# Kernel tuning notes

Hardware: AMD Instinct MI355X
Metric: run time of the kernel (lower is better)

## Reference

```python
import jax, jax.numpy as jnp
import numpy as np

PATCH = 8
MASK_RATIO = 0.75
B, H, W, C = 64, 512, 512, 3
NPH, NPW = H // PATCH, W // PATCH          # 64, 64
NP_TOT = NPH * NPW                          # 4096
NUM_MASK = int(NP_TOT * MASK_RATIO)         # 3072


def setup_inputs() -> dict:
    key = jax.random.key(0)
    k_img, k_perm = jax.random.split(key)
    images = jax.random.normal(k_img, (B, H, W, C), dtype=jnp.float32)
    # random-without-replacement masked patch indices per image (tf.random.shuffle(idx)[:num_mask])
    perm_keys = jax.random.split(k_perm, B)
    perms = jax.vmap(lambda k: jax.random.permutation(k, NP_TOT))(perm_keys)
    mask_indices = perms[:, :NUM_MASK].astype(jnp.int32)  # [B, NUM_MASK]
    return {"images": images, "mask_indices": mask_indices}


def reference(images, mask_indices):
    # Build per-image flat patch mask: ones with zeros scattered at mask_indices.
    b = images.shape[0]
    mask_flat = jnp.ones((b, NP_TOT), dtype=images.dtype)
    mask_flat = mask_flat.at[jnp.arange(b)[:, None], mask_indices].set(0.0)
    # [B, NPH, NPW] -> nearest-neighbor upsample to [B, H, W, 1] by patch repetition
    mask = mask_flat.reshape(b, NPH, NPW)
    mask = jnp.repeat(jnp.repeat(mask, PATCH, axis=1), PATCH, axis=2)[..., None]
    return images * mask
```

## Files before the change

kernel.cpp:

```cpp
#include <hip/hip_runtime.h>

#define BATCH    64
#define HEIGHT   512
#define WIDTH    512
#define CHAN     3
#define PATCH    8
#define NPH      64
#define NPW      64
#define NP_TOT   4096
#define NUM_MASK 3072

#define PER_IMG4 (HEIGHT * WIDTH * CHAN / 4)
#define PER_ROW4 (WIDTH * CHAN / 4)
#define TOTAL4   (BATCH * PER_IMG4)

typedef float f32x4 __attribute__((ext_vector_type(4)));

__global__ __launch_bounds__(256) void rm_build_mask(
        const int* __restrict__ mask_indices,
        unsigned char* __restrict__ mask) {
    const int b = blockIdx.x;
    const int t = threadIdx.x;

    uint4 ones = make_uint4(0x01010101u, 0x01010101u, 0x01010101u, 0x01010101u);
    reinterpret_cast<uint4*>(mask + b * NP_TOT)[t] = ones;
    __syncthreads();

    const int* __restrict__ idx = mask_indices + b * NUM_MASK;
    unsigned char* __restrict__ m = mask + b * NP_TOT;
#pragma unroll
    for (int j = 0; j < 12; ++j) {
        m[idx[t + j * 256]] = (unsigned char)0;
    }
}

__global__ __launch_bounds__(256) void rm_apply_mask(
        const f32x4* __restrict__ in,
        f32x4* __restrict__ out,
        const unsigned char* __restrict__ mask) {
    const int tid = blockIdx.x * blockDim.x + threadIdx.x;
    const int b  = tid / PER_IMG4;
    const int r  = tid - b * PER_IMG4;
    const int y  = r / PER_ROW4;
    const int x4 = r - y * PER_ROW4;
    const int px = x4 / 6;
    const int py = y >> 3;
    const unsigned char m = mask[b * NP_TOT + (py << 6) + px];
    f32x4 v = (f32x4)(0.f, 0.f, 0.f, 0.f);
    if (m) v = __builtin_nontemporal_load(&in[tid]);
    __builtin_nontemporal_store(v, &out[tid]);
}

extern "C" void kernel_launch(void* const* d_in, const int* in_sizes, int n_in,
                              void* d_out, int out_size, void* d_ws, size_t ws_size,
                              hipStream_t stream) {
    const float* images       = (const float*)d_in[0];
    const int*   mask_indices = (const int*)d_in[1];
    float*       out          = (float*)d_out;
    unsigned char* mask       = (unsigned char*)d_ws;

    rm_build_mask<<<BATCH, 256, 0, stream>>>(mask_indices, mask);

    rm_apply_mask<<<TOTAL4 / 256, 256, 0, stream>>>(
        (const f32x4*)images, (f32x4*)out, mask);
}
```

Measured before the change: 312.0 us.

## Fuse mask build into apply kernel with per-strip shared-memory mask

Replaces the two-kernel pipeline (global byte-mask build, then apply) with one kernel. Each block covers one 8-row strip of one image. It builds that strip's 64-entry patch mask in shared memory by scanning all 3072 indices of the image, then conditionally loads and stores 12 float4s per thread. This removes a kernel launch and the global mask round-trip. In exchange, each block rereads the full 12KB index list, which adds 64x redundant index traffic per image.

```diff
diff --git a/kernel.cpp b/kernel.cpp
--- a/kernel.cpp
+++ b/kernel.cpp
@@ -12,43 +12,49 @@
 
 #define PER_IMG4 (HEIGHT * WIDTH * CHAN / 4)
 #define PER_ROW4 (WIDTH * CHAN / 4)
+#define STRIP4   (PATCH * PER_ROW4)
 #define TOTAL4   (BATCH * PER_IMG4)
 
 typedef float f32x4 __attribute__((ext_vector_type(4)));
 
-__global__ __launch_bounds__(256) void rm_build_mask(
-        const int* __restrict__ mask_indices,
-        unsigned char* __restrict__ mask) {
-    const int b = blockIdx.x;
-    const int t = threadIdx.x;
+__global__ __launch_bounds__(256) void rm_fused(
+        const int*  __restrict__ mask_indices,
+        const f32x4* __restrict__ in,
+        f32x4*       __restrict__ out) {
+    const int blk = blockIdx.x;
+    const int b   = blk >> 6;
+    const int py  = blk & 63;
+    const int t   = threadIdx.x;
 
-    uint4 ones = make_uint4(0x01010101u, 0x01010101u, 0x01010101u, 0x01010101u);
-    reinterpret_cast<uint4*>(mask + b * NP_TOT)[t] = ones;
+    __shared__ unsigned char sm[NPW];
+
+    if (t < NPW) sm[t] = (unsigned char)1;
     __syncthreads();
 
-    const int* __restrict__ idx = mask_indices + b * NUM_MASK;
-    unsigned char* __restrict__ m = mask + b * NP_TOT;
+    const int4* __restrict__ idx4 =
+        reinterpret_cast<const int4*>(mask_indices + b * NUM_MASK);
+    const int lo = py << 6;
+#pragma unroll
+    for (int k = 0; k < 3; ++k) {
+        int4 v = idx4[t + 256 * k];
+        int d;
+        d = v.x - lo; if ((unsigned)d < (unsigned)NPW) sm[d] = (unsigned char)0;
+        d = v.y - lo; if ((unsigned)d < (unsigned)NPW) sm[d] = (unsigned char)0;
+        d = v.z - lo; if ((unsigned)d < (unsigned)NPW) sm[d] = (unsigned char)0;
+        d = v.w - lo; if ((unsigned)d < (unsigned)NPW) sm[d] = (unsigned char)0;
+    }
+    __syncthreads();
+
+    const int strip_base = b * PER_IMG4 + py * STRIP4;
 #pragma unroll
     for (int j = 0; j < 12; ++j) {
-        m[idx[t + j * 256]] = (unsigned char)0;
+        const int r  = j * 256 + t;
+        const int x4 = r % PER_ROW4;
+        const int px = x4 / 6;
+        f32x4 v = (f32x4)(0.f, 0.f, 0.f, 0.f);
+        if (sm[px]) v = __builtin_nontemporal_load(&in[strip_base + r]);
+        __builtin_nontemporal_store(v, &out[strip_base + r]);
     }
-}
-
-__global__ __launch_bounds__(256) void rm_apply_mask(
-        const f32x4* __restrict__ in,
-        f32x4* __restrict__ out,
-        const unsigned char* __restrict__ mask) {
-    const int tid = blockIdx.x * blockDim.x + threadIdx.x;
-    const int b  = tid / PER_IMG4;
-    const int r  = tid - b * PER_IMG4;
-    const int y  = r / PER_ROW4;
-    const int x4 = r - y * PER_ROW4;
-    const int px = x4 / 6;
-    const int py = y >> 3;
-    const unsigned char m = mask[b * NP_TOT + (py << 6) + px];
-    f32x4 v = (f32x4)(0.f, 0.f, 0.f, 0.f);
-    if (m) v = __builtin_nontemporal_load(&in[tid]);
-    __builtin_nontemporal_store(v, &out[tid]);
 }
 
 extern "C" void kernel_launch(void* const* d_in, const int* in_sizes, int n_in,
@@ -57,10 +63,8 @@
     const float* images       = (const float*)d_in[0];
     const int*   mask_indices = (const int*)d_in[1];
     float*       out          = (float*)d_out;
-    unsigned char* mask       = (unsigned char*)d_ws;
+    (void)d_ws; (void)ws_size;
 
-    rm_build_mask<<<BATCH, 256, 0, stream>>>(mask_indices, mask);
-
-    rm_apply_mask<<<TOTAL4 / 256, 256, 0, stream>>>(
-        (const f32x4*)images, (f32x4*)out, mask);
+    rm_fused<<<BATCH * NPH, 256, 0, stream>>>(
+        mask_indices, (const f32x4*)images, (f32x4*)out);
 }
```

Result: no change. 313.2 us (+0.4%).
